# Kernel optimization log

Hardware: AMD Instinct MI355X
Metric: run time of the kernel (lower is better)

The kernel has to match this reference:

```python
import jax, jax.numpy as jnp
import numpy as np

M, IN, OUT = 8192, 4096, 4096
BITWIDTH = 7


def psto_shift_int32(x, shift):
    """Pseudo-stochastic right-shift of int32 x by `shift` bits -> int8.
    Faithful to PstoShiftInt32: floor-divide, derive a pseudo random number
    from the low half of the remainder, compare against the high half."""
    pow_s = jnp.left_shift(jnp.int32(1), shift)
    rt = jnp.floor_divide(x, pow_s)
    prob = jnp.abs(x - rt * pow_s)
    half_pow = jnp.left_shift(jnp.int32(1), shift // 2)
    qp = jnp.floor_divide(prob, half_pow)
    prn = prob - qp * half_pow
    prn = jnp.where(shift % 2 == 1, prn * 2, prn)
    dec = jnp.where(qp <= prn, jnp.int32(0), jnp.int32(1)) * jnp.sign(x)
    return jnp.clip(rt + dec, -127, 127).astype(jnp.int8)


def range_bitwidth(x):
    # RangeEstimate: ceil(log2(max|x|)), 0 if all-zero (torch also goes via float)
    m = jnp.max(jnp.abs(x)).astype(jnp.float32)
    return jnp.where(m == 0, jnp.int32(0), jnp.ceil(jnp.log2(m)).astype(jnp.int32))


def act_calc(acc, exp_in):
    """Shift int32 accumulator back to int8 and track the block exponent."""
    bw = range_bitwidth(acc)
    shift = bw - BITWIDTH
    # shift>1 -> shift by `shift`; shift==1 -> shift by 2; else -> plain int8 cast
    eff = jnp.where(shift > 1, shift, jnp.where(shift == 1, jnp.int32(2), jnp.int32(0)))
    rounded = psto_shift_int32(acc, jnp.maximum(eff, 0))
    out = jnp.where(eff > 0, rounded, acc.astype(jnp.int8))  # int8 cast wraps, as in torch
    exp_out = (exp_in + eff).astype(jnp.int8)
    return out, exp_out


def setup_inputs() -> dict:
    key = jax.random.key(0)
    k1, k2 = jax.random.split(key)
    # int8-valued tensors kept in int32 containers for the matmul accumulate
    act_in = jax.random.randint(k1, (M, IN), -127, 128, dtype=jnp.int32)
    weight = jax.random.randint(k2, (OUT, IN), -127, 128, dtype=jnp.int32)
    return {"act_in": act_in, "exp_in": -6, "weight": weight, "weight_exp": -9}


def reference(act_in, exp_in, weight, weight_exp):
    # the roundoff4 padding in the original is a no-op)
    acc = jnp.matmul(act_in, weight.T)  # [M, OUT] int32
    act_out, exp_out = act_calc(acc, jnp.int32(exp_in) + jnp.int32(weight_exp))
    return act_out, exp_out
```

## Files before the change

### kernel.cpp

```cpp
#include <hip/hip_runtime.h>
#include <stdint.h>
#include <math.h>

#define M_DIM 8192
#define N_DIM 4096
#define K_DIM 4096
#define BITWIDTH 7

#define BM 128
#define BN 128
#define BK 64

using i32x4 = __attribute__((ext_vector_type(4))) int;

__global__ __launch_bounds__(256) void pack_kernel(const int* __restrict__ src,
                                                   uint32_t* __restrict__ dst,
                                                   int n4) {
    int i = blockIdx.x * blockDim.x + threadIdx.x;
    if (i >= n4) return;
    int4 v = ((const int4*)src)[i];
    uint32_t p = (uint32_t)(v.x & 0xFF)
               | ((uint32_t)(v.y & 0xFF) << 8)
               | ((uint32_t)(v.z & 0xFF) << 16)
               | ((uint32_t)(v.w & 0xFF) << 24);
    dst[i] = p;
}

__device__ __forceinline__ void gload_lds16(const int8_t* g, int8_t* lds) {
    __builtin_amdgcn_global_load_lds(
        (__attribute__((address_space(1))) void*)g,
        (__attribute__((address_space(3))) void*)lds,
        16, 0, 0);
}

__global__ __launch_bounds__(256) void gemm_i8(const int8_t* __restrict__ A8,
                                               const int8_t* __restrict__ B8,
                                               int* __restrict__ C,
                                               int* __restrict__ maxabs) {
    __shared__ __align__(16) int8_t As[BM * BK];
    __shared__ __align__(16) int8_t Bs[BN * BK];
    __shared__ int wmaxs[4];

    const int tid  = threadIdx.x;
    const int wave = tid >> 6;
    const int lane = tid & 63;

    const int row0 = blockIdx.y * BM;
    const int col0 = blockIdx.x * BN;

    const int wm = (wave >> 1) * 64;
    const int wn = (wave & 1) * 64;

    i32x4 acc[4][4];
#pragma unroll
    for (int i = 0; i < 4; ++i)
#pragma unroll
        for (int j = 0; j < 4; ++j)
            acc[i][j] = (i32x4)(0);

    const int lr  = lane >> 2;
    const int lcb = (lane & 3) << 4;
    const int ra  = wave * 32;

    const int8_t* ag = A8 + (size_t)(row0 + ra + lr) * K_DIM + lcb;
    const int8_t* bg = B8 + (size_t)(col0 + ra + lr) * K_DIM + lcb;

    const int fr = lane & 15;
    const int fk = (lane >> 4) << 4;

    for (int k0 = 0; k0 < K_DIM; k0 += BK) {
        __syncthreads();
        gload_lds16(ag + k0,                        As + ra * BK);
        gload_lds16(ag + k0 + (size_t)16 * K_DIM,   As + (ra + 16) * BK);
        gload_lds16(bg + k0,                        Bs + ra * BK);
        gload_lds16(bg + k0 + (size_t)16 * K_DIM,   Bs + (ra + 16) * BK);
        __syncthreads();

        i32x4 af[4], bf[4];
#pragma unroll
        for (int i = 0; i < 4; ++i)
            af[i] = *(const i32x4*)(As + (wm + i * 16 + fr) * BK + fk);
#pragma unroll
        for (int j = 0; j < 4; ++j)
            bf[j] = *(const i32x4*)(Bs + (wn + j * 16 + fr) * BK + fk);

#pragma unroll
        for (int i = 0; i < 4; ++i)
#pragma unroll
            for (int j = 0; j < 4; ++j)
                acc[i][j] = __builtin_amdgcn_mfma_i32_16x16x64_i8(
                    af[i], bf[j], acc[i][j], 0, 0, 0);
    }

    int mymax = 0;
    const int crow = (lane >> 4) << 2;
    const int ccol = lane & 15;
#pragma unroll
    for (int i = 0; i < 4; ++i) {
#pragma unroll
        for (int j = 0; j < 4; ++j) {
            int* p = C + (size_t)(row0 + wm + i * 16 + crow) * N_DIM
                       + (col0 + wn + j * 16 + ccol);
#pragma unroll
            for (int r = 0; r < 4; ++r) {
                int v = acc[i][j][r];
                p[(size_t)r * N_DIM] = v;
                int a = v < 0 ? -v : v;
                mymax = a > mymax ? a : mymax;
            }
        }
    }

#pragma unroll
    for (int off = 32; off > 0; off >>= 1) {
        int o = __shfl_down(mymax, off, 64);
        mymax = o > mymax ? o : mymax;
    }
    if (lane == 0) wmaxs[wave] = mymax;
    __syncthreads();
    if (tid == 0) {
        int bmx = wmaxs[0];
        for (int w = 1; w < 4; ++w) bmx = wmaxs[w] > bmx ? wmaxs[w] : bmx;
        atomicMax(maxabs, bmx);
    }
}

__device__ __forceinline__ int psto(int x, int eff) {
    if (eff > 0) {
        int rt   = x >> eff;
        int prob = x & ((1 << eff) - 1);
        int h    = eff >> 1;
        int qp   = prob >> h;
        int prn  = (prob & ((1 << h) - 1)) << (eff & 1);
        int sgn  = (x > 0) - (x < 0);
        int r    = rt + ((qp <= prn) ? 0 : sgn);
        r = r < -127 ? -127 : r;
        r = r > 127 ? 127 : r;
        return r;
    }
    return (int)(int8_t)x;
}

__global__ __launch_bounds__(256) void finalize_kernel(int* __restrict__ C,
        const int* __restrict__ maxabs,
        const int* __restrict__ exp_in,
        const int* __restrict__ wexp) {
    const int m = *maxabs;
    int bw = 0;
    if (m != 0) bw = (int)ceilf(log2f((float)m));
    const int shift = bw - BITWIDTH;
    const int eff = (shift > 1) ? shift : ((shift == 1) ? 2 : 0);

    const size_t idx = ((size_t)blockIdx.x * blockDim.x + threadIdx.x) * 4;
    int4 v = *(const int4*)(C + idx);
    int4 o;
    o.x = psto(v.x, eff);
    o.y = psto(v.y, eff);
    o.z = psto(v.z, eff);
    o.w = psto(v.w, eff);
    *(int4*)(C + idx) = o;

    if (idx == 0) {
        C[(size_t)M_DIM * N_DIM] = (int)(int8_t)(exp_in[0] + wexp[0] + eff);
    }
}

extern "C" void kernel_launch(void* const* d_in, const int* in_sizes, int n_in,
                              void* d_out, int out_size, void* d_ws, size_t ws_size,
                              hipStream_t stream) {
    const int* act    = (const int*)d_in[0];
    const int* exp_in = (const int*)d_in[1];
    const int* wt     = (const int*)d_in[2];
    const int* wexp   = (const int*)d_in[3];

    int8_t* act8   = (int8_t*)d_ws;
    int8_t* w8     = act8 + (size_t)M_DIM * K_DIM;
    int*    maxabs = (int*)(w8 + (size_t)N_DIM * K_DIM);

    hipMemsetAsync(maxabs, 0, sizeof(int), stream);

    pack_kernel<<<(M_DIM * K_DIM / 4) / 256, 256, 0, stream>>>(
        act, (uint32_t*)act8, M_DIM * K_DIM / 4);
    pack_kernel<<<(N_DIM * K_DIM / 4) / 256, 256, 0, stream>>>(
        wt, (uint32_t*)w8, N_DIM * K_DIM / 4);

    int* C = (int*)d_out;
    dim3 grid(N_DIM / BN, M_DIM / BM);
    gemm_i8<<<grid, 256, 0, stream>>>(act8, w8, C, maxabs);

    finalize_kernel<<<((size_t)M_DIM * N_DIM / 4) / 256, 256, 0, stream>>>(
        C, maxabs, exp_in, wexp);
}
```

Before: 495.4 us.

## Use 32x32x32 int8 MFMA, merge pack kernels, widen finalize per thread

The GEMM moves from 16x16x64 to 32x32x32 int8 MFMA tiles. Each wave now holds 2x2 accumulators of 16 ints, and the LDS fragment loads and output store indexing are rewritten to match. The two pack launches become one kernel where each thread packs 8 elements, and finalize handles 8 elements per thread. Together these aim to cut MFMA issue and LDS read overhead, launch count, and per-thread overhead in the memory-bound kernels. The catch is a more scattered store pattern for C and a change in register pressure.

```diff
diff --git a/kernel.cpp b/kernel.cpp
--- a/kernel.cpp
+++ b/kernel.cpp
@@ -11,19 +11,25 @@
 #define BN 128
 #define BK 64
 
-using i32x4 = __attribute__((ext_vector_type(4))) int;
-
-__global__ __launch_bounds__(256) void pack_kernel(const int* __restrict__ src,
-                                                   uint32_t* __restrict__ dst,
-                                                   int n4) {
+using i32x4  = __attribute__((ext_vector_type(4)))  int;
+using i32x16 = __attribute__((ext_vector_type(16))) int;
+
+__global__ __launch_bounds__(256) void pack_both_kernel(
+        const int* __restrict__ act, const int* __restrict__ wt,
+        uint32_t* __restrict__ act8, uint32_t* __restrict__ w8) {
+    const int ACT_N8 = (M_DIM * K_DIM) / 8;
     int i = blockIdx.x * blockDim.x + threadIdx.x;
-    if (i >= n4) return;
-    int4 v = ((const int4*)src)[i];
-    uint32_t p = (uint32_t)(v.x & 0xFF)
-               | ((uint32_t)(v.y & 0xFF) << 8)
-               | ((uint32_t)(v.z & 0xFF) << 16)
-               | ((uint32_t)(v.w & 0xFF) << 24);
-    dst[i] = p;
+    const int* src;
+    uint32_t* dst;
+    if (i < ACT_N8) { src = act; dst = act8; }
+    else            { src = wt;  dst = w8;  i -= ACT_N8; }
+    int4 a = ((const int4*)src)[2 * i];
+    int4 b = ((const int4*)src)[2 * i + 1];
+    uint32_t p0 = (uint32_t)(a.x & 0xFF) | ((uint32_t)(a.y & 0xFF) << 8)
+                | ((uint32_t)(a.z & 0xFF) << 16) | ((uint32_t)(a.w & 0xFF) << 24);
+    uint32_t p1 = (uint32_t)(b.x & 0xFF) | ((uint32_t)(b.y & 0xFF) << 8)
+                | ((uint32_t)(b.z & 0xFF) << 16) | ((uint32_t)(b.w & 0xFF) << 24);
+    ((uint2*)dst)[i] = make_uint2(p0, p1);
 }
 
 __device__ __forceinline__ void gload_lds16(const int8_t* g, int8_t* lds) {
@@ -51,12 +57,12 @@
     const int wm = (wave >> 1) * 64;
     const int wn = (wave & 1) * 64;
 
-    i32x4 acc[4][4];
-#pragma unroll
-    for (int i = 0; i < 4; ++i)
-#pragma unroll
-        for (int j = 0; j < 4; ++j)
-            acc[i][j] = (i32x4)(0);
+    i32x16 acc[2][2];
+#pragma unroll
+    for (int i = 0; i < 2; ++i)
+#pragma unroll
+        for (int j = 0; j < 2; ++j)
+            acc[i][j] = (i32x16)(0);
 
     const int lr  = lane >> 2;
     const int lcb = (lane & 3) << 4;
@@ -65,8 +71,8 @@
     const int8_t* ag = A8 + (size_t)(row0 + ra + lr) * K_DIM + lcb;
     const int8_t* bg = B8 + (size_t)(col0 + ra + lr) * K_DIM + lcb;
 
-    const int fr = lane & 15;
-    const int fk = (lane >> 4) << 4;
+    const int fr = lane & 31;
+    const int fk = (lane >> 5) << 4;
 
     for (int k0 = 0; k0 < K_DIM; k0 += BK) {
         __syncthreads();
@@ -76,35 +82,39 @@
         gload_lds16(bg + k0 + (size_t)16 * K_DIM,   Bs + (ra + 16) * BK);
         __syncthreads();
 
-        i32x4 af[4], bf[4];
-#pragma unroll
-        for (int i = 0; i < 4; ++i)
-            af[i] = *(const i32x4*)(As + (wm + i * 16 + fr) * BK + fk);
-#pragma unroll
-        for (int j = 0; j < 4; ++j)
-            bf[j] = *(const i32x4*)(Bs + (wn + j * 16 + fr) * BK + fk);
-
-#pragma unroll
-        for (int i = 0; i < 4; ++i)
-#pragma unroll
-            for (int j = 0; j < 4; ++j)
-                acc[i][j] = __builtin_amdgcn_mfma_i32_16x16x64_i8(
-                    af[i], bf[j], acc[i][j], 0, 0, 0);
+        i32x4 af[2][2], bf[2][2];
+#pragma unroll
+        for (int i = 0; i < 2; ++i)
+#pragma unroll
+            for (int kk = 0; kk < 2; ++kk) {
+                af[i][kk] = *(const i32x4*)(As + (wm + i * 32 + fr) * BK + kk * 32 + fk);
+                bf[i][kk] = *(const i32x4*)(Bs + (wn + i * 32 + fr) * BK + kk * 32 + fk);
+            }
+
+#pragma unroll
+        for (int kk = 0; kk < 2; ++kk)
+#pragma unroll
+            for (int i = 0; i < 2; ++i)
+#pragma unroll
+                for (int j = 0; j < 2; ++j)
+                    acc[i][j] = __builtin_amdgcn_mfma_i32_32x32x32_i8(
+                        af[i][kk], bf[j][kk], acc[i][j], 0, 0, 0);
     }
 
     int mymax = 0;
-    const int crow = (lane >> 4) << 2;
-    const int ccol = lane & 15;
-#pragma unroll
-    for (int i = 0; i < 4; ++i) {
-#pragma unroll
-        for (int j = 0; j < 4; ++j) {
-            int* p = C + (size_t)(row0 + wm + i * 16 + crow) * N_DIM
-                       + (col0 + wn + j * 16 + ccol);
-#pragma unroll
-            for (int r = 0; r < 4; ++r) {
+    const int ccol = lane & 31;
+    const int rbase = (lane >> 5) << 2;
+#pragma unroll
+    for (int i = 0; i < 2; ++i) {
+#pragma unroll
+        for (int j = 0; j < 2; ++j) {
+            int* p = C + (size_t)(row0 + wm + i * 32) * N_DIM
+                       + (col0 + wn + j * 32 + ccol);
+#pragma unroll
+            for (int r = 0; r < 16; ++r) {
+                int row = (r & 3) + 8 * (r >> 2) + rbase;
                 int v = acc[i][j][r];
-                p[(size_t)r * N_DIM] = v;
+                p[(size_t)row * N_DIM] = v;
                 int a = v < 0 ? -v : v;
                 mymax = a > mymax ? a : mymax;
             }
@@ -151,14 +161,16 @@
     const int shift = bw - BITWIDTH;
     const int eff = (shift > 1) ? shift : ((shift == 1) ? 2 : 0);
 
-    const size_t idx = ((size_t)blockIdx.x * blockDim.x + threadIdx.x) * 4;
-    int4 v = *(const int4*)(C + idx);
-    int4 o;
-    o.x = psto(v.x, eff);
-    o.y = psto(v.y, eff);
-    o.z = psto(v.z, eff);
-    o.w = psto(v.w, eff);
-    *(int4*)(C + idx) = o;
+    const size_t idx = ((size_t)blockIdx.x * blockDim.x + threadIdx.x) * 8;
+    int4 v0 = *(const int4*)(C + idx);
+    int4 v1 = *(const int4*)(C + idx + 4);
+    int4 o0, o1;
+    o0.x = psto(v0.x, eff); o0.y = psto(v0.y, eff);
+    o0.z = psto(v0.z, eff); o0.w = psto(v0.w, eff);
+    o1.x = psto(v1.x, eff); o1.y = psto(v1.y, eff);
+    o1.z = psto(v1.z, eff); o1.w = psto(v1.w, eff);
+    *(int4*)(C + idx) = o0;
+    *(int4*)(C + idx + 4) = o1;
 
     if (idx == 0) {
         C[(size_t)M_DIM * N_DIM] = (int)(int8_t)(exp_in[0] + wexp[0] + eff);
@@ -179,15 +191,13 @@
 
     hipMemsetAsync(maxabs, 0, sizeof(int), stream);
 
-    pack_kernel<<<(M_DIM * K_DIM / 4) / 256, 256, 0, stream>>>(
-        act, (uint32_t*)act8, M_DIM * K_DIM / 4);
-    pack_kernel<<<(N_DIM * K_DIM / 4) / 256, 256, 0, stream>>>(
-        wt, (uint32_t*)w8, N_DIM * K_DIM / 4);
+    pack_both_kernel<<<24576, 256, 0, stream>>>(
+        act, wt, (uint32_t*)act8, (uint32_t*)w8);
 
     int* C = (int*)d_out;
     dim3 grid(N_DIM / BN, M_DIM / BM);
     gemm_i8<<<grid, 256, 0, stream>>>(act8, w8, C, maxabs);
 
-    finalize_kernel<<<((size_t)M_DIM * N_DIM / 4) / 256, 256, 0, stream>>>(
+    finalize_kernel<<<((size_t)M_DIM * N_DIM / 8) / 256, 256, 0, stream>>>(
         C, maxabs, exp_in, wexp);
 }
```

Result: no change. 490.6 us (-1.0%).
